# Kernel optimization log

Measured on AMD Instinct MI355X. Metric: run time of the kernel, lower is better.

The kernel has to match this reference:

```python
import jax, jax.numpy as jnp
import numpy as np

N_CLASSES = 19
N_BINS = 10
EPS = 1e-13


def setup_inputs() -> dict:
    key = jax.random.key(0)
    k1, k2 = jax.random.split(key)
    output = jax.random.normal(k1, (1, N_CLASSES, 1024, 2048), dtype=jnp.float32)
    target = jax.random.randint(k2, (1, 1024, 2048), 0, N_CLASSES, dtype=jnp.int32)
    return {"output": output, "target": target}


def reference(output, target):
    # output: [B, C, H, W] logits; target: [B, H, W] int labels
    B, C, H, W = output.shape
    p = jax.nn.softmax(output, axis=1)  # [B, C, H, W]

    # Bin i covers (i/N_BINS, (i+1)/N_BINS]; p == 0 belongs to no bin.
    bin_idx = jnp.clip(jnp.ceil(p * N_BINS).astype(jnp.int32) - 1, 0, N_BINS - 1)
    valid = p > 0

    cls = jnp.arange(C, dtype=jnp.int32)[None, :, None, None]  # idealMap per class
    # Combined (class, bin) segment id; invalid pixels dumped into extra segment.
    seg = jnp.where(valid, cls * N_BINS + bin_idx, C * N_BINS).reshape(-1)
    n_seg = C * N_BINS + 1

    p_flat = p.reshape(-1)
    conf_sum = jax.ops.segment_sum(p_flat, seg, num_segments=n_seg)[:-1].reshape(C, N_BINS)
    no_pred = jax.ops.segment_sum(jnp.ones_like(p_flat), seg, num_segments=n_seg)[:-1].reshape(C, N_BINS)
    correct = (target[:, None, :, :] == cls).astype(p.dtype)  # idealMap == target
    no_acc = jax.ops.segment_sum(correct.reshape(-1), seg, num_segments=n_seg)[:-1].reshape(C, N_BINS)

    avg_acc = no_acc / (no_pred + EPS)
    avg_conf = conf_sum / (no_pred + EPS)
    loss = jnp.sum((avg_acc - avg_conf) ** 2 * (no_pred / jnp.sum(no_pred)))
    return loss
```

## Files before the change

### kernel.cpp

```cpp
#include <hip/hip_runtime.h>

#define NC 19
#define NB 10
#define NCELL (NC * NB)
#define NPART (3 * NCELL + 2 * NC)
#define REP 4
#define NSLOT 16
#define TPB 256
#define TILE 256
#define NROWS (NC + 1)
#define BLOCKS 768

__device__ __forceinline__ void load16_lds(const void* g, void* l) {
    auto* gp = reinterpret_cast<const unsigned int __attribute__((address_space(1)))*>(
        reinterpret_cast<uintptr_t>(g));
    auto* lp = reinterpret_cast<unsigned int __attribute__((address_space(3)))*>(
        reinterpret_cast<uintptr_t>(l));
    __builtin_amdgcn_global_load_lds(gp, lp, 16, 0, 0);
}

__global__ __launch_bounds__(TPB, 3) void cce_pass1(
    const float* __restrict__ logits, const int* __restrict__ tgt,
    float* __restrict__ gacc, int hw)
{
    constexpr int O_CONF = 0;
    constexpr int O_PRED = REP * NCELL;
    constexpr int O_ACC  = 2 * REP * NCELL;
    constexpr int O_PSUM = 3 * REP * NCELL;
    constexpr int O_INV  = 3 * REP * NCELL + REP * NC;
    constexpr int LDS_N  = O_INV + NC;

    __shared__ float buf[2][NROWS][TILE];
    __shared__ float hist[LDS_N];

    for (int i = threadIdx.x; i < LDS_N; i += TPB) hist[i] = 0.0f;
    __syncthreads();

    const int lane = threadIdx.x & 63;
    const int wv   = threadIdx.x >> 6;
    const int rep  = threadIdx.x & (REP - 1);
    const int p    = threadIdx.x;

    float psum[NC];
#pragma unroll
    for (int c = 0; c < NC; ++c) psum[c] = 0.0f;

    const int ntiles = hw / TILE;
    const int stride = (int)gridDim.x;

    auto stage = [&](int b, int t) {
#pragma unroll
        for (int r5 = 0; r5 < 5; ++r5) {
            const int row = wv * 5 + r5;
            const void* g = (row < NC)
                ? (const void*)(logits + (size_t)row * hw + (size_t)t * TILE + lane * 4)
                : (const void*)(tgt + (size_t)t * TILE + lane * 4);
            load16_lds(g, (void*)&buf[b][row][0]);
        }
    };

    const int t0 = (int)blockIdx.x;
    if (t0 < ntiles) stage(0, t0);
    int cur = 0;

    for (int t = t0; t < ntiles; t += stride) {
        const int nxt = t + stride;
        if (nxt < ntiles) {
            stage(cur ^ 1, nxt);
            asm volatile("s_waitcnt vmcnt(5)" ::: "memory");
        } else {
            asm volatile("s_waitcnt vmcnt(0)" ::: "memory");
        }
        __builtin_amdgcn_s_barrier();
        asm volatile("" ::: "memory");

        float x[NC];
#pragma unroll
        for (int c = 0; c < NC; ++c) x[c] = buf[cur][c][p];
        const int tg = ((const int*)&buf[cur][NC][0])[p];

        float m = x[0];
#pragma unroll
        for (int c = 1; c < NC; ++c) m = fmaxf(m, x[c]);
        float s = 0.0f;
#pragma unroll
        for (int c = 0; c < NC; ++c) { x[c] = __expf(x[c] - m); s += x[c]; }
        const float r = __builtin_amdgcn_rcpf(s);

        float pt = 0.0f, pmin = 1.0f;
#pragma unroll
        for (int c = 0; c < NC; ++c) {
            const float pv = x[c] * r;
            psum[c] += pv;
            if (c == tg) pt = pv;
            pmin = fminf(pmin, pv);
            const float q = pv * 10.0f;
            if (q > 1.0f) {
                int bb = (int)ceilf(q) - 1; bb = bb > NB - 1 ? NB - 1 : bb;
                atomicAdd(&hist[O_CONF + rep * NCELL + c * NB + bb], pv);
                atomicAdd(&hist[O_PRED + rep * NCELL + c * NB + bb], 1.0f);
            }
        }
        if (pt > 0.0f) {
            int bb = (int)ceilf(pt * 10.0f) - 1;
            bb = bb < 0 ? 0 : (bb > NB - 1 ? NB - 1 : bb);
            atomicAdd(&hist[O_ACC + rep * NCELL + tg * NB + bb], 1.0f);
        }
        if (!(pmin > 0.0f)) {
#pragma unroll
            for (int c = 0; c < NC; ++c)
                if (!(x[c] * r > 0.0f)) atomicAdd(&hist[O_INV + c], 1.0f);
        }

        asm volatile("" ::: "memory");
        __builtin_amdgcn_s_barrier();
        cur ^= 1;
    }

#pragma unroll
    for (int c = 0; c < NC; ++c)
        atomicAdd(&hist[O_PSUM + rep * NC + c], psum[c]);
    __syncthreads();

    float* slot = gacc + (size_t)(blockIdx.x & (NSLOT - 1)) * NPART;
    for (int j = threadIdx.x; j < NPART; j += TPB) {
        float v = 0.0f;
        if (j < NCELL) {
            for (int rr = 0; rr < REP; ++rr) v += hist[O_CONF + rr * NCELL + j];
        } else if (j < 2 * NCELL) {
            for (int rr = 0; rr < REP; ++rr) v += hist[O_PRED + rr * NCELL + (j - NCELL)];
        } else if (j < 3 * NCELL) {
            for (int rr = 0; rr < REP; ++rr) v += hist[O_ACC + rr * NCELL + (j - 2 * NCELL)];
        } else if (j < 3 * NCELL + NC) {
            for (int rr = 0; rr < REP; ++rr) v += hist[O_PSUM + rr * NC + (j - 3 * NCELL)];
        } else {
            v = hist[O_INV + (j - 3 * NCELL - NC)];
        }
        atomicAdd(&slot[j], v);
    }
}

__global__ void cce_pass2(const float* __restrict__ gacc, float* __restrict__ out, int hw)
{
    __shared__ double fin[NPART];
    const int j = threadIdx.x;
    if (j < NPART) {
        double v = 0.0;
        for (int s = 0; s < NSLOT; ++s) v += (double)gacc[(size_t)s * NPART + j];
        fin[j] = v;
    }
    __syncthreads();

    if (j < NC) {
        double spred = 0.0, sconf = 0.0;
        for (int b = 1; b < NB; ++b) {
            spred += fin[NCELL + j * NB + b];
            sconf += fin[j * NB + b];
        }
        const double validc = (double)hw - fin[3 * NCELL + NC + j];
        fin[NCELL + j * NB] = validc - spred;
        fin[j * NB]         = fin[3 * NCELL + j] - sconf;
    }
    __syncthreads();

    if (j < 64) {
        double tot = 0.0;
        for (int c = j; c < NCELL; c += 64) tot += fin[NCELL + c];
#pragma unroll
        for (int o = 32; o > 0; o >>= 1) tot += __shfl_down(tot, o);
        tot = __shfl(tot, 0);

        double loss = 0.0;
        for (int c = j; c < NCELL; c += 64) {
            const double pred = fin[NCELL + c];
            const double conf = fin[c];
            const double acc  = fin[2 * NCELL + c];
            const double d    = (acc - conf) / (pred + 1e-13);
            loss += d * d * (pred / tot);
        }
#pragma unroll
        for (int o = 32; o > 0; o >>= 1) loss += __shfl_down(loss, o);
        if (j == 0) out[0] = (float)loss;
    }
}

extern "C" void kernel_launch(void* const* d_in, const int* in_sizes, int n_in,
                              void* d_out, int out_size, void* d_ws, size_t ws_size,
                              hipStream_t stream)
{
    const float* logits = (const float*)d_in[0];
    const int*   tgt    = (const int*)d_in[1];
    float*       gacc   = (float*)d_ws;
    const int    hw     = in_sizes[1];

    hipMemsetAsync(gacc, 0, (size_t)NSLOT * NPART * sizeof(float), stream);
    cce_pass1<<<BLOCKS, TPB, 0, stream>>>(logits, tgt, gacc, hw);
    cce_pass2<<<1, 640, 0, stream>>>(gacc, (float*)d_out, hw);
}
```

Before: 271.6 us.

## Give each wave private double-buffered LDS tiles and branchless dump-slot histogram atomics

```diff
diff --git a/kernel.cpp b/kernel.cpp
--- a/kernel.cpp
+++ b/kernel.cpp
@@ -5,21 +5,22 @@
 #define NCELL (NC * NB)
 #define NPART (3 * NCELL + 2 * NC)
 #define REP 4
-#define NSLOT 16
+#define NSLOT 32
 #define TPB 256
 #define TILE 256
+#define WTILE 64
 #define NROWS (NC + 1)
-#define BLOCKS 768
+#define BLOCKS 512
 
-__device__ __forceinline__ void load16_lds(const void* g, void* l) {
+__device__ __forceinline__ void load4_lds(const void* g, void* l) {
     auto* gp = reinterpret_cast<const unsigned int __attribute__((address_space(1)))*>(
         reinterpret_cast<uintptr_t>(g));
     auto* lp = reinterpret_cast<unsigned int __attribute__((address_space(3)))*>(
         reinterpret_cast<uintptr_t>(l));
-    __builtin_amdgcn_global_load_lds(gp, lp, 16, 0, 0);
+    __builtin_amdgcn_global_load_lds(gp, lp, 4, 0, 0);
 }
 
-__global__ __launch_bounds__(TPB, 3) void cce_pass1(
+__global__ __launch_bounds__(TPB) void cce_pass1(
     const float* __restrict__ logits, const int* __restrict__ tgt,
     float* __restrict__ gacc, int hw)
 {
@@ -27,10 +28,11 @@
     constexpr int O_PRED = REP * NCELL;
     constexpr int O_ACC  = 2 * REP * NCELL;
     constexpr int O_PSUM = 3 * REP * NCELL;
-    constexpr int O_INV  = 3 * REP * NCELL + REP * NC;
-    constexpr int LDS_N  = O_INV + NC;
+    constexpr int O_INV  = O_PSUM + REP * NC;
+    constexpr int O_DUMP = O_INV + NC;
+    constexpr int LDS_N  = O_DUMP + TPB;
 
-    __shared__ float buf[2][NROWS][TILE];
+    __shared__ float wbuf[4][2][NROWS][WTILE];
     __shared__ float hist[LDS_N];
 
     for (int i = threadIdx.x; i < LDS_N; i += TPB) hist[i] = 0.0f;
@@ -38,46 +40,44 @@
 
     const int lane = threadIdx.x & 63;
     const int wv   = threadIdx.x >> 6;
-    const int rep  = threadIdx.x & (REP - 1);
-    const int p    = threadIdx.x;
+    const int rep  = lane & (REP - 1);
+    const int dl   = O_DUMP + threadIdx.x;
 
     float psum[NC];
 #pragma unroll
     for (int c = 0; c < NC; ++c) psum[c] = 0.0f;
 
     const int ntiles = hw / TILE;
-    const int stride = (int)gridDim.x;
+    const int nt     = (ntiles + (int)gridDim.x - 1) / (int)gridDim.x;
+    const int start  = (int)blockIdx.x * nt;
+    const int end    = (start + nt) < ntiles ? (start + nt) : ntiles;
 
     auto stage = [&](int b, int t) {
 #pragma unroll
-        for (int r5 = 0; r5 < 5; ++r5) {
-            const int row = wv * 5 + r5;
-            const void* g = (row < NC)
-                ? (const void*)(logits + (size_t)row * hw + (size_t)t * TILE + lane * 4)
-                : (const void*)(tgt + (size_t)t * TILE + lane * 4);
-            load16_lds(g, (void*)&buf[b][row][0]);
+        for (int rr = 0; rr < NROWS; ++rr) {
+            const void* g = (rr < NC)
+                ? (const void*)(logits + (size_t)rr * hw + (size_t)t * TILE + wv * WTILE + lane)
+                : (const void*)(tgt + (size_t)t * TILE + wv * WTILE + lane);
+            load4_lds(g, (void*)&wbuf[wv][b][rr][0]);
         }
     };
 
-    const int t0 = (int)blockIdx.x;
-    if (t0 < ntiles) stage(0, t0);
     int cur = 0;
+    if (start < end) stage(0, start);
 
-    for (int t = t0; t < ntiles; t += stride) {
-        const int nxt = t + stride;
-        if (nxt < ntiles) {
-            stage(cur ^ 1, nxt);
-            asm volatile("s_waitcnt vmcnt(5)" ::: "memory");
+    for (int t = start; t < end; ++t) {
+        if (t + 1 < end) {
+            stage(cur ^ 1, t + 1);
+            asm volatile("s_waitcnt vmcnt(20)" ::: "memory");
         } else {
             asm volatile("s_waitcnt vmcnt(0)" ::: "memory");
         }
-        __builtin_amdgcn_s_barrier();
-        asm volatile("" ::: "memory");
+        __builtin_amdgcn_sched_barrier(0);
 
         float x[NC];
 #pragma unroll
-        for (int c = 0; c < NC; ++c) x[c] = buf[cur][c][p];
-        const int tg = ((const int*)&buf[cur][NC][0])[p];
+        for (int c = 0; c < NC; ++c) x[c] = wbuf[wv][cur][c][lane];
+        const int tg = ((const int*)&wbuf[wv][cur][NC][0])[lane];
 
         float m = x[0];
 #pragma unroll
@@ -90,30 +90,26 @@
         float pt = 0.0f, pmin = 1.0f;
 #pragma unroll
         for (int c = 0; c < NC; ++c) {
-            const float pv = x[c] * r;
-            psum[c] += pv;
-            if (c == tg) pt = pv;
-            pmin = fminf(pmin, pv);
-            const float q = pv * 10.0f;
-            if (q > 1.0f) {
-                int bb = (int)ceilf(q) - 1; bb = bb > NB - 1 ? NB - 1 : bb;
-                atomicAdd(&hist[O_CONF + rep * NCELL + c * NB + bb], pv);
-                atomicAdd(&hist[O_PRED + rep * NCELL + c * NB + bb], 1.0f);
-            }
+            const float p = x[c] * r;
+            psum[c] += p;
+            pt   = (c == tg) ? p : pt;
+            pmin = fminf(pmin, p);
+            int bb = (int)ceilf(p * 10.0f) - 1;
+            const bool hot = bb > 0;
+            bb = bb > NB - 1 ? NB - 1 : bb;
+            const int cell = rep * NCELL + c * NB + bb;
+            atomicAdd(&hist[hot ? O_CONF + cell : dl], p);
+            atomicAdd(&hist[hot ? O_PRED + cell : dl], 1.0f);
         }
-        if (pt > 0.0f) {
-            int bb = (int)ceilf(pt * 10.0f) - 1;
-            bb = bb < 0 ? 0 : (bb > NB - 1 ? NB - 1 : bb);
-            atomicAdd(&hist[O_ACC + rep * NCELL + tg * NB + bb], 1.0f);
-        }
+        int bt = (int)ceilf(pt * 10.0f) - 1;
+        bt = bt < 0 ? 0 : (bt > NB - 1 ? NB - 1 : bt);
+        atomicAdd(&hist[(pt > 0.0f) ? O_ACC + rep * NCELL + tg * NB + bt : dl], 1.0f);
+
         if (!(pmin > 0.0f)) {
 #pragma unroll
             for (int c = 0; c < NC; ++c)
                 if (!(x[c] * r > 0.0f)) atomicAdd(&hist[O_INV + c], 1.0f);
         }
-
-        asm volatile("" ::: "memory");
-        __builtin_amdgcn_s_barrier();
         cur ^= 1;
     }
 
```

Result: slower. 606.2 us (+123.2%).

## Replace double-buffered grid-stride loop with single-buffer contiguous tiles of 512 pixels

Applied to the files above, without the earlier changes.

```diff
diff --git a/kernel.cpp b/kernel.cpp
--- a/kernel.cpp
+++ b/kernel.cpp
@@ -5,11 +5,11 @@
 #define NCELL (NC * NB)
 #define NPART (3 * NCELL + 2 * NC)
 #define REP 4
-#define NSLOT 16
+#define NSLOT 32
 #define TPB 256
-#define TILE 256
+#define TILE 512
 #define NROWS (NC + 1)
-#define BLOCKS 768
+#define BLOCKS 1024
 
 __device__ __forceinline__ void load16_lds(const void* g, void* l) {
     auto* gp = reinterpret_cast<const unsigned int __attribute__((address_space(1)))*>(
@@ -19,7 +19,7 @@
     __builtin_amdgcn_global_load_lds(gp, lp, 16, 0, 0);
 }
 
-__global__ __launch_bounds__(TPB, 3) void cce_pass1(
+__global__ __launch_bounds__(TPB) void cce_pass1(
     const float* __restrict__ logits, const int* __restrict__ tgt,
     float* __restrict__ gacc, int hw)
 {
@@ -27,10 +27,10 @@
     constexpr int O_PRED = REP * NCELL;
     constexpr int O_ACC  = 2 * REP * NCELL;
     constexpr int O_PSUM = 3 * REP * NCELL;
-    constexpr int O_INV  = 3 * REP * NCELL + REP * NC;
+    constexpr int O_INV  = O_PSUM + REP * NC;
     constexpr int LDS_N  = O_INV + NC;
 
-    __shared__ float buf[2][NROWS][TILE];
+    __shared__ float buf[NROWS][TILE];
     __shared__ float hist[LDS_N];
 
     for (int i = threadIdx.x; i < LDS_N; i += TPB) hist[i] = 0.0f;
@@ -39,82 +39,77 @@
     const int lane = threadIdx.x & 63;
     const int wv   = threadIdx.x >> 6;
     const int rep  = threadIdx.x & (REP - 1);
-    const int p    = threadIdx.x;
 
     float psum[NC];
 #pragma unroll
     for (int c = 0; c < NC; ++c) psum[c] = 0.0f;
 
     const int ntiles = hw / TILE;
-    const int stride = (int)gridDim.x;
+    const int nt     = ntiles / (int)gridDim.x;
+    const int start  = (int)blockIdx.x * nt;
+    const int end    = start + nt;
 
-    auto stage = [&](int b, int t) {
+    for (int t = start; t < end; ++t) {
 #pragma unroll
         for (int r5 = 0; r5 < 5; ++r5) {
             const int row = wv * 5 + r5;
-            const void* g = (row < NC)
-                ? (const void*)(logits + (size_t)row * hw + (size_t)t * TILE + lane * 4)
-                : (const void*)(tgt + (size_t)t * TILE + lane * 4);
-            load16_lds(g, (void*)&buf[b][row][0]);
+#pragma unroll
+            for (int i = 0; i < 2; ++i) {
+                const void* g = (row < NC)
+                    ? (const void*)(logits + (size_t)row * hw + (size_t)t * TILE + i * 256 + lane * 4)
+                    : (const void*)(tgt + (size_t)t * TILE + i * 256 + lane * 4);
+                load16_lds(g, (void*)&buf[row][i * 256]);
+            }
         }
-    };
-
-    const int t0 = (int)blockIdx.x;
-    if (t0 < ntiles) stage(0, t0);
-    int cur = 0;
-
-    for (int t = t0; t < ntiles; t += stride) {
-        const int nxt = t + stride;
-        if (nxt < ntiles) {
-            stage(cur ^ 1, nxt);
-            asm volatile("s_waitcnt vmcnt(5)" ::: "memory");
-        } else {
-            asm volatile("s_waitcnt vmcnt(0)" ::: "memory");
-        }
+        asm volatile("s_waitcnt vmcnt(0)" ::: "memory");
         __builtin_amdgcn_s_barrier();
         asm volatile("" ::: "memory");
 
-        float x[NC];
 #pragma unroll
-        for (int c = 0; c < NC; ++c) x[c] = buf[cur][c][p];
-        const int tg = ((const int*)&buf[cur][NC][0])[p];
+        for (int pp = 0; pp < 2; ++pp) {
+            const int p = threadIdx.x + pp * TPB;
 
-        float m = x[0];
+            float x[NC];
 #pragma unroll
-        for (int c = 1; c < NC; ++c) m = fmaxf(m, x[c]);
-        float s = 0.0f;
+            for (int c = 0; c < NC; ++c) x[c] = buf[c][p];
+            const int tg = ((const int*)&buf[NC][0])[p];
+
+            float m = x[0];
 #pragma unroll
-        for (int c = 0; c < NC; ++c) { x[c] = __expf(x[c] - m); s += x[c]; }
-        const float r = __builtin_amdgcn_rcpf(s);
+            for (int c = 1; c < NC; ++c) m = fmaxf(m, x[c]);
+            float s = 0.0f;
+#pragma unroll
+            for (int c = 0; c < NC; ++c) { x[c] = __expf(x[c] - m); s += x[c]; }
+            const float r = __builtin_amdgcn_rcpf(s);
 
-        float pt = 0.0f, pmin = 1.0f;
+            float pt = 0.0f, pmin = 1.0f;
 #pragma unroll
-        for (int c = 0; c < NC; ++c) {
-            const float pv = x[c] * r;
-            psum[c] += pv;
-            if (c == tg) pt = pv;
-            pmin = fminf(pmin, pv);
-            const float q = pv * 10.0f;
-            if (q > 1.0f) {
-                int bb = (int)ceilf(q) - 1; bb = bb > NB - 1 ? NB - 1 : bb;
-                atomicAdd(&hist[O_CONF + rep * NCELL + c * NB + bb], pv);
-                atomicAdd(&hist[O_PRED + rep * NCELL + c * NB + bb], 1.0f);
+            for (int c = 0; c < NC; ++c) {
+                const float pv = x[c] * r;
+                psum[c] += pv;
+                pt   = (c == tg) ? pv : pt;
+                pmin = fminf(pmin, pv);
+                int bb = (int)ceilf(pv * 10.0f) - 1;
+                if (bb > 0) {
+                    bb = bb > NB - 1 ? NB - 1 : bb;
+                    atomicAdd(&hist[O_CONF + rep * NCELL + c * NB + bb], pv);
+                    atomicAdd(&hist[O_PRED + rep * NCELL + c * NB + bb], 1.0f);
+                }
             }
-        }
-        if (pt > 0.0f) {
-            int bb = (int)ceilf(pt * 10.0f) - 1;
-            bb = bb < 0 ? 0 : (bb > NB - 1 ? NB - 1 : bb);
-            atomicAdd(&hist[O_ACC + rep * NCELL + tg * NB + bb], 1.0f);
-        }
-        if (!(pmin > 0.0f)) {
+            if (pt > 0.0f) {
+                int bt = (int)ceilf(pt * 10.0f) - 1;
+                bt = bt < 0 ? 0 : (bt > NB - 1 ? NB - 1 : bt);
+                atomicAdd(&hist[O_ACC + rep * NCELL + tg * NB + bt], 1.0f);
+            }
+            if (!(pmin > 0.0f)) {
 #pragma unroll
-            for (int c = 0; c < NC; ++c)
-                if (!(x[c] * r > 0.0f)) atomicAdd(&hist[O_INV + c], 1.0f);
+                for (int c = 0; c < NC; ++c)
+                    if (!(x[c] * r > 0.0f)) atomicAdd(&hist[O_INV + c], 1.0f);
+            }
         }
 
         asm volatile("" ::: "memory");
         __builtin_amdgcn_s_barrier();
-        cur ^= 1;
     }
 
 #pragma unroll
```

After: 281.3 us. 3.6% more time.
